# Optimization experiments

Hardware: AMD Instinct MI355X
Metric: run time of the kernel (lower is better)

Reference implementation:

```python
import jax, jax.numpy as jnp
import numpy as np

H = 16  # headNum
D = 1024  # d_model
DK = D // H


def setup_inputs() -> dict:
    key = jax.random.key(0)
    ks = jax.random.split(key, 11)
    B, S = 2, 2048
    scale = 1.0 / np.sqrt(D)
    inp = {
        'query': jax.random.normal(ks[0], (B, S, D), jnp.float32),
        'key':   jax.random.normal(ks[1], (B, S, D), jnp.float32),
        'value': jax.random.normal(ks[2], (B, S, D), jnp.float32),
        # nn.Linear params: W is [out, in], y = x @ W.T + b
        'Wq': jax.random.normal(ks[3], (D, D), jnp.float32) * scale,
        'bq': jnp.zeros((D,), jnp.float32),
        'Wk': jax.random.normal(ks[4], (D, D), jnp.float32) * scale,
        'bk': jnp.zeros((D,), jnp.float32),
        'Wv': jax.random.normal(ks[5], (D, D), jnp.float32) * scale,
        'bv': jnp.zeros((D,), jnp.float32),
        'Wo': jax.random.normal(ks[6], (D, D), jnp.float32) * scale,
        'bo': jnp.zeros((D,), jnp.float32),
    }
    return inp


def reference(query, key, value, Wq, bq, Wk, bk, Wv, bv, Wo, bo):
    B, S, _ = query.shape
    # projections (torch Linear: x @ W.T + b), split heads -> [B, H, S, DK]
    q = (query @ Wq.T + bq).reshape(B, S, H, DK).transpose(0, 2, 1, 3)
    k = (key   @ Wk.T + bk).reshape(B, S, H, DK).transpose(0, 2, 1, 3)
    v = (value @ Wv.T + bv).reshape(B, S, H, DK).transpose(0, 2, 1, 3)
    # scores [B, H, S, S] = Q K^T / sqrt(d_k)  (fully materialized, as in source)
    scores = jnp.einsum('bhqd,bhkd->bhqk', q, k) * (DK ** -0.5)
    p_attn = jax.nn.softmax(scores, axis=-1)  # dropout = identity (eval)
    x = jnp.einsum('bhqk,bhkd->bhqd', p_attn, v)
    x = x.transpose(0, 2, 1, 3).reshape(B, S, H * DK)
    return x @ Wo.T + bo
```

## Files before the change

kernel.cpp:

```cpp
#include <hip/hip_runtime.h>

#define BATCH 2
#define SEQ   2048
#define NH    16
#define DK    64
#define DM    1024
#define MROWS 4096
#define NX    4194304
#define NW    1048576

typedef __attribute__((ext_vector_type(8))) short bf16x8;
typedef __attribute__((ext_vector_type(4))) short bf16x4;
typedef __attribute__((ext_vector_type(4))) float f32x4;
typedef __attribute__((ext_vector_type(4))) unsigned short us16x4;
typedef __attribute__((ext_vector_type(2))) unsigned int u32x2;

#if __has_builtin(__builtin_amdgcn_mfma_f32_16x16x16bf16_1k)
#define MFMA16(a, b, c) __builtin_amdgcn_mfma_f32_16x16x16bf16_1k(a, b, c, 0, 0, 0)
#else
#define MFMA16(a, b, c) (c)
#endif

__device__ __forceinline__ unsigned short f2bf(float f) {
  unsigned int u = __builtin_bit_cast(unsigned int, f);
  u += 0x7FFFu + ((u >> 16) & 1u);
  return (unsigned short)(u >> 16);
}

__device__ __forceinline__ unsigned int pkbf(float hi, float lo) {
#if __has_builtin(__builtin_amdgcn_perm)
  return __builtin_amdgcn_perm(__builtin_bit_cast(unsigned int, hi),
                               __builtin_bit_cast(unsigned int, lo), 0x07060302u);
#else
  return (__builtin_bit_cast(unsigned int, hi) & 0xffff0000u) |
         (__builtin_bit_cast(unsigned int, lo) >> 16);
#endif
}

__device__ __forceinline__ void g2l16(void* lds, const void* g) {
  __builtin_amdgcn_global_load_lds(
      (const __attribute__((address_space(1))) void*)g,
      (__attribute__((address_space(3))) void*)lds, 16, 0, 0);
}

__global__ __launch_bounds__(256) void cast_all(
    const float* __restrict__ q, const float* __restrict__ k, const float* __restrict__ v,
    const float* __restrict__ wq, const float* __restrict__ wk,
    const float* __restrict__ wv, const float* __restrict__ wo,
    unsigned short* __restrict__ dst) {
  size_t e = ((size_t)blockIdx.x * 256 + threadIdx.x) * 4;
  const float* src;
  if      (e < (size_t)NX)        src = q  + e;
  else if (e < (size_t)2*NX)      src = k  + (e - (size_t)NX);
  else if (e < (size_t)3*NX)      src = v  + (e - (size_t)2*NX);
  else if (e < (size_t)3*NX+NW)   src = wq + (e - (size_t)3*NX);
  else if (e < (size_t)3*NX+2*NW) src = wk + (e - (size_t)3*NX-NW);
  else if (e < (size_t)3*NX+3*NW) src = wv + (e - (size_t)3*NX-2*NW);
  else                            src = wo + (e - (size_t)3*NX-3*NW);
  float4 f = *(const float4*)src;
  us16x4 o;
  o[0] = f2bf(f.x); o[1] = f2bf(f.y); o[2] = f2bf(f.z); o[3] = f2bf(f.w);
  *(us16x4*)(dst + e) = o;
}

template <int MODE, int BM>
__global__ __launch_bounds__(256) void gemm_bt(
    const unsigned short* __restrict__ Xbase, const unsigned short* __restrict__ Wbase,
    const float* __restrict__ b0, const float* __restrict__ b1, const float* __restrict__ b2,
    unsigned short* __restrict__ qkv_dst, float* __restrict__ fout, float qscale) {
  constexpr int IM = BM / 32;
  constexpr int ASHOTS = (BM * 32) / 2048;
  const int tid  = threadIdx.x;
  const int lane = tid & 63;
  const int w    = tid >> 6;
  const int wm   = w >> 1, wn = w & 1;
  const int x15  = lane & 15, quad = lane >> 4;
  const int row0 = blockIdx.x * BM;
  const int col0 = blockIdx.y * 128;
  const int z    = blockIdx.z;

  const unsigned short* A  = Xbase + (size_t)z * NX;
  const unsigned short* Wp = Wbase + (size_t)z * NW;
  const float* bias = (MODE == 0) ? (z == 0 ? b0 : (z == 1 ? b1 : b2)) : b0;
  const float zs = (MODE == 0 && z == 0) ? qscale : 1.0f;

  __shared__ __align__(16) unsigned short At[2][BM * 32];
  __shared__ __align__(16) unsigned short Bt[2][128 * 32];

  f32x4 acc[IM][4] = {};

  auto stage = [&](int buf, int kt) {
#pragma unroll
    for (int j = 0; j < ASHOTS; ++j) {
      int e = (j * 256 + tid) * 8;
      int r = e >> 5, c = e & 31;
      g2l16(&At[buf][e], A + (size_t)(row0 + r) * DM + kt + c);
    }
#pragma unroll
    for (int j = 0; j < 2; ++j) {
      int e = (j * 256 + tid) * 8;
      int r = e >> 5, c = e & 31;
      g2l16(&Bt[buf][e], Wp + (size_t)(col0 + r) * DM + kt + c);
    }
  };

  stage(0, 0);
  for (int it = 0; it < DM / 32; ++it) {
    const int cur = it & 1;
    __syncthreads();
    if (it + 1 < DM / 32) stage(cur ^ 1, (it + 1) * 32);
    bf16x8 af[IM], bfv[4];
#pragma unroll
    for (int i = 0; i < IM; ++i)
      af[i] = *(const bf16x8*)&At[cur][(wm * (BM / 2) + i * 16 + x15) * 32 + quad * 8];
#pragma unroll
    for (int jn = 0; jn < 4; ++jn)
      bfv[jn] = *(const bf16x8*)&Bt[cur][(wn * 64 + jn * 16 + x15) * 32 + quad * 8];
#pragma unroll
    for (int i = 0; i < IM; ++i)
#pragma unroll
      for (int jn = 0; jn < 4; ++jn)
        acc[i][jn] = __builtin_amdgcn_mfma_f32_16x16x32_bf16(af[i], bfv[jn], acc[i][jn], 0, 0, 0);
  }

#pragma unroll
  for (int jn = 0; jn < 4; ++jn) {
    const int n = col0 + wn * 64 + jn * 16 + x15;
    const float bv = bias[n];
#pragma unroll
    for (int i = 0; i < IM; ++i) {
      const int m0 = row0 + wm * (BM / 2) + i * 16 + quad * 4;
      if (MODE == 0 && z == 2) {
        us16x4 pk;
#pragma unroll
        for (int r = 0; r < 4; ++r) pk[r] = f2bf(acc[i][jn][r] + bv);
        const int b = m0 >> 11, s = m0 & 2047;
        const int h = n >> 6,  dk = n & 63;
        *(us16x4*)&qkv_dst[(size_t)2 * NX + (((size_t)(b * NH + h) * DK + dk) << 11) + s] = pk;
      } else {
#pragma unroll
        for (int r = 0; r < 4; ++r) {
          const int m = m0 + r;
          float val = (acc[i][jn][r] + bv) * zs;
          if (MODE == 0) {
            const int b = m >> 11, s = m & 2047;
            const int h = n >> 6,  dk = n & 63;
            qkv_dst[(size_t)z * NX + (((size_t)(b * NH + h) * SEQ + s) << 6) + dk] = f2bf(val);
          } else {
            fout[(size_t)m * DM + n] = val;
          }
        }
      }
    }
  }
}

__global__ __launch_bounds__(256) void attn(
    const unsigned short* __restrict__ Qb, const unsigned short* __restrict__ Kb,
    const unsigned short* __restrict__ VTb, unsigned short* __restrict__ AO) {
  const int tid  = threadIdx.x;
  const int lane = tid & 63;
  const int w    = tid >> 6;
  const int x15  = lane & 15, quad = lane >> 4;
  const int qt = blockIdx.x;
  const int h  = blockIdx.y;
  const int b  = blockIdx.z;
  const size_t bh = ((size_t)(b * NH + h)) * SEQ * DK;
  const unsigned short* Q  = Qb  + bh;
  const unsigned short* K  = Kb  + bh;
  const unsigned short* VT = VTb + bh;
  const int q0 = qt * 64 + w * 16;

  __shared__ __align__(16) unsigned short Kl[2][64 * 64];
  __shared__ __align__(16) unsigned short Vl[2][64 * 64];

  bf16x8 qf[2];
#pragma unroll
  for (int ks = 0; ks < 2; ++ks)
    qf[ks] = *(const bf16x8*)&Q[(size_t)(q0 + x15) * DK + ks * 32 + quad * 8];

  f32x4 po[4] = {};
  f32x4 pol = {};
  const bf16x4 vone = {(short)0x3F80, (short)0x3F80, (short)0x3F80, (short)0x3F80};

  const int sK0 = tid >> 3,          sK1 = (tid + 256) >> 3;
  const int dgK0 = (tid & 7) ^ (sK0 & 7), dgK1 = (tid & 7) ^ (sK1 & 7);

  auto stageKV = [&](int buf, int s0) {
    g2l16(&Kl[buf][(size_t)tid * 8],         K + (size_t)(s0 + sK0) * DK + dgK0 * 8);
    g2l16(&Kl[buf][(size_t)(tid + 256) * 8], K + (size_t)(s0 + sK1) * DK + dgK1 * 8);
    g2l16(&Vl[buf][(size_t)tid * 8],         VT + (size_t)sK0 * SEQ + s0 + dgK0 * 8);
    g2l16(&Vl[buf][(size_t)(tid + 256) * 8], VT + (size_t)sK1 * SEQ + s0 + dgK1 * 8);
  };

  stageKV(0, 0);
  for (int s0 = 0; s0 < SEQ; s0 += 64) {
    const int cur = (s0 >> 6) & 1;
    __syncthreads();
    if (s0 + 64 < SEQ) stageKV(cur ^ 1, s0 + 64);

    bf16x8 kf[4][2];
#pragma unroll
    for (int sh = 0; sh < 4; ++sh) {
      const int kbase = (sh * 16 + x15) * 8;
      kf[sh][0] = *(const bf16x8*)&Kl[cur][(kbase + ((0 + quad) ^ (x15 & 7))) * 8];
      kf[sh][1] = *(const bf16x8*)&Kl[cur][(kbase + ((4 + quad) ^ (x15 & 7))) * 8];
    }

#pragma unroll
    for (int sh = 0; sh < 4; ++sh) {
      f32x4 sacc = {};
      sacc = __builtin_amdgcn_mfma_f32_16x16x32_bf16(kf[sh][0], qf[0], sacc, 0, 0, 0);
      sacc = __builtin_amdgcn_mfma_f32_16x16x32_bf16(kf[sh][1], qf[1], sacc, 0, 0, 0);
      float p0 = __builtin_amdgcn_exp2f(sacc[0]);
      float p1 = __builtin_amdgcn_exp2f(sacc[1]);
      float p2 = __builtin_amdgcn_exp2f(sacc[2]);
      float p3 = __builtin_amdgcn_exp2f(sacc[3]);
      u32x2 uu;
      uu[0] = pkbf(p1, p0);
      uu[1] = pkbf(p3, p2);
      bf16x4 pf = __builtin_bit_cast(bf16x4, uu);
      pol = MFMA16(vone, pf, pol);

#pragma unroll
      for (int nt = 0; nt < 4; ++nt) {
        const int d = nt * 16 + x15;
        const int sg = (sh * 2 + (quad >> 1)) ^ (d & 7);
        bf16x4 vf = *(const bf16x4*)&Vl[cur][(d * 8 + sg) * 8 + (quad & 1) * 4];
        po[nt] = MFMA16(vf, pf, po[nt]);
      }
    }
  }

  const float inv = 1.0f / pol[0];
  const int s = q0 + x15;
#pragma unroll
  for (int nt = 0; nt < 4; ++nt) {
    us16x4 pk;
#pragma unroll
    for (int r = 0; r < 4; ++r) pk[r] = f2bf(po[nt][r] * inv);
    const int d = nt * 16 + quad * 4;
    *(us16x4*)&AO[((size_t)(b * SEQ + s)) * DM + h * DK + d] = pk;
  }
}

extern "C" void kernel_launch(void* const* d_in, const int* in_sizes, int n_in,
                              void* d_out, int out_size, void* d_ws, size_t ws_size,
                              hipStream_t stream) {
  const float* q  = (const float*)d_in[0];
  const float* k  = (const float*)d_in[1];
  const float* v  = (const float*)d_in[2];
  const float* wq = (const float*)d_in[3];
  const float* bq = (const float*)d_in[4];
  const float* wk = (const float*)d_in[5];
  const float* bk = (const float*)d_in[6];
  const float* wv = (const float*)d_in[7];
  const float* bv = (const float*)d_in[8];
  const float* wo = (const float*)d_in[9];
  const float* bo = (const float*)d_in[10];
  float* out = (float*)d_out;

  unsigned short* ws = (unsigned short*)d_ws;
  unsigned short* Xq = ws;
  unsigned short* Wb = ws + (size_t)3 * NX;
  unsigned short* Qb = ws + (size_t)3 * NX + 4 * NW;
  unsigned short* AO = Qb + (size_t)3 * NX;

  const float qscale = 0.125f * 1.4426950408889634f;

  cast_all<<<16384, 256, 0, stream>>>(q, k, v, wq, wk, wv, wo, ws);
  gemm_bt<0, 128><<<dim3(32, 8, 3), 256, 0, stream>>>(Xq, Wb, bq, bk, bv, Qb, nullptr, qscale);
  attn<<<dim3(32, 16, 2), 256, 0, stream>>>(Qb, Qb + (size_t)NX, Qb + (size_t)2 * NX, AO);
  gemm_bt<1, 64><<<dim3(64, 8, 1), 256, 0, stream>>>(AO, Wb + (size_t)3 * NW, bo, bo, bo,
                                                     nullptr, out, 1.0f);
}
```

Measured before the change: 234.0 us.

## Fuse fp32-to-bf16 activation cast into QKV GEMM A-tile staging

The separate cast of query/key/value to bf16 is removed. The QKV projection GEMM now reads fp32 activations into registers, converts them with a packed bf16 convert, and writes them into LDS after the MFMA block, so the next tile's load overlaps compute. This avoids writing and re-reading about 24MB of bf16 activations in an extra pass, at the cost of register-staged loads in place of direct global-to-LDS loads, and double the global A traffic per tile. The attention kernel also precomputes its swizzled LDS offsets to cut per-iteration index arithmetic.

```diff
diff --git a/kernel.cpp b/kernel.cpp
--- a/kernel.cpp
+++ b/kernel.cpp
@@ -27,6 +27,16 @@
   return (unsigned short)(u >> 16);
 }
 
+__device__ __forceinline__ unsigned int cvt2bf(float a, float b) {
+#if __has_builtin(__builtin_amdgcn_cvt_pk_bf16_f32)
+  typedef __attribute__((ext_vector_type(2))) __bf16 bf16v2;
+  bf16v2 v = __builtin_amdgcn_cvt_pk_bf16_f32(a, b);
+  return __builtin_bit_cast(unsigned int, v);
+#else
+  return (unsigned int)f2bf(a) | ((unsigned int)f2bf(b) << 16);
+#endif
+}
+
 __device__ __forceinline__ unsigned int pkbf(float hi, float lo) {
 #if __has_builtin(__builtin_amdgcn_perm)
   return __builtin_amdgcn_perm(__builtin_bit_cast(unsigned int, hi),
@@ -43,56 +53,143 @@
       (__attribute__((address_space(3))) void*)lds, 16, 0, 0);
 }
 
-__global__ __launch_bounds__(256) void cast_all(
-    const float* __restrict__ q, const float* __restrict__ k, const float* __restrict__ v,
+__global__ __launch_bounds__(256) void cast_w(
     const float* __restrict__ wq, const float* __restrict__ wk,
     const float* __restrict__ wv, const float* __restrict__ wo,
     unsigned short* __restrict__ dst) {
   size_t e = ((size_t)blockIdx.x * 256 + threadIdx.x) * 4;
   const float* src;
-  if      (e < (size_t)NX)        src = q  + e;
-  else if (e < (size_t)2*NX)      src = k  + (e - (size_t)NX);
-  else if (e < (size_t)3*NX)      src = v  + (e - (size_t)2*NX);
-  else if (e < (size_t)3*NX+NW)   src = wq + (e - (size_t)3*NX);
-  else if (e < (size_t)3*NX+2*NW) src = wk + (e - (size_t)3*NX-NW);
-  else if (e < (size_t)3*NX+3*NW) src = wv + (e - (size_t)3*NX-2*NW);
-  else                            src = wo + (e - (size_t)3*NX-3*NW);
+  if      (e < (size_t)NW)     src = wq + e;
+  else if (e < (size_t)2*NW)   src = wk + (e - (size_t)NW);
+  else if (e < (size_t)3*NW)   src = wv + (e - (size_t)2*NW);
+  else                         src = wo + (e - (size_t)3*NW);
   float4 f = *(const float4*)src;
   us16x4 o;
   o[0] = f2bf(f.x); o[1] = f2bf(f.y); o[2] = f2bf(f.z); o[3] = f2bf(f.w);
   *(us16x4*)(dst + e) = o;
 }
 
-template <int MODE, int BM>
-__global__ __launch_bounds__(256) void gemm_bt(
-    const unsigned short* __restrict__ Xbase, const unsigned short* __restrict__ Wbase,
-    const float* __restrict__ b0, const float* __restrict__ b1, const float* __restrict__ b2,
-    unsigned short* __restrict__ qkv_dst, float* __restrict__ fout, float qscale) {
-  constexpr int IM = BM / 32;
-  constexpr int ASHOTS = (BM * 32) / 2048;
+__global__ __launch_bounds__(256) void gemm_qkv(
+    const float* __restrict__ Xq, const float* __restrict__ Xk, const float* __restrict__ Xv,
+    const unsigned short* __restrict__ Wb,
+    const float* __restrict__ bq, const float* __restrict__ bk, const float* __restrict__ bv,
+    unsigned short* __restrict__ dst, float qscale) {
   const int tid  = threadIdx.x;
   const int lane = tid & 63;
   const int w    = tid >> 6;
   const int wm   = w >> 1, wn = w & 1;
   const int x15  = lane & 15, quad = lane >> 4;
-  const int row0 = blockIdx.x * BM;
+  const int row0 = blockIdx.x * 128;
   const int col0 = blockIdx.y * 128;
   const int z    = blockIdx.z;
 
-  const unsigned short* A  = Xbase + (size_t)z * NX;
-  const unsigned short* Wp = Wbase + (size_t)z * NW;
-  const float* bias = (MODE == 0) ? (z == 0 ? b0 : (z == 1 ? b1 : b2)) : b0;
-  const float zs = (MODE == 0 && z == 0) ? qscale : 1.0f;
-
-  __shared__ __align__(16) unsigned short At[2][BM * 32];
+  const float* X = (z == 0) ? Xq : (z == 1 ? Xk : Xv);
+  const unsigned short* Wp = Wb + (size_t)z * NW;
+  const float* bias = (z == 0) ? bq : (z == 1 ? bk : bv);
+  const float zs = (z == 0) ? qscale : 1.0f;
+
+  __shared__ __align__(16) unsigned short At[2][128 * 32];
   __shared__ __align__(16) unsigned short Bt[2][128 * 32];
 
-  f32x4 acc[IM][4] = {};
+  f32x4 acc[4][4] = {};
+  float4 xa[4];
+
+  auto loadA = [&](int kt) {
+#pragma unroll
+    for (int j = 0; j < 4; ++j) {
+      int e = (j * 256 + tid) * 4;
+      int r = e >> 5, c = e & 31;
+      xa[j] = *(const float4*)&X[(size_t)(row0 + r) * DM + kt + c];
+    }
+  };
+  auto writeA = [&](int buf) {
+#pragma unroll
+    for (int j = 0; j < 4; ++j) {
+      int e = (j * 256 + tid) * 4;
+      u32x2 p;
+      p[0] = cvt2bf(xa[j].x, xa[j].y);
+      p[1] = cvt2bf(xa[j].z, xa[j].w);
+      *(u32x2*)&At[buf][e] = p;
+    }
+  };
+  auto stageB = [&](int buf, int kt) {
+#pragma unroll
+    for (int j = 0; j < 2; ++j) {
+      int e = (j * 256 + tid) * 8;
+      int r = e >> 5, c = e & 31;
+      g2l16(&Bt[buf][e], Wp + (size_t)(col0 + r) * DM + kt + c);
+    }
+  };
+
+  loadA(0);
+  stageB(0, 0);
+  writeA(0);
+  for (int it = 0; it < DM / 32; ++it) {
+    const int cur = it & 1;
+    __syncthreads();
+    const bool nxt = (it + 1 < DM / 32);
+    if (nxt) { loadA((it + 1) * 32); stageB(cur ^ 1, (it + 1) * 32); }
+    bf16x8 af[4], bfv[4];
+#pragma unroll
+    for (int i = 0; i < 4; ++i) {
+      af[i]  = *(const bf16x8*)&At[cur][(wm * 64 + i * 16 + x15) * 32 + quad * 8];
+      bfv[i] = *(const bf16x8*)&Bt[cur][(wn * 64 + i * 16 + x15) * 32 + quad * 8];
+    }
+#pragma unroll
+    for (int i = 0; i < 4; ++i)
+#pragma unroll
+      for (int jn = 0; jn < 4; ++jn)
+        acc[i][jn] = __builtin_amdgcn_mfma_f32_16x16x32_bf16(af[i], bfv[jn], acc[i][jn], 0, 0, 0);
+    if (nxt) writeA(cur ^ 1);
+  }
+
+#pragma unroll
+  for (int jn = 0; jn < 4; ++jn) {
+    const int n = col0 + wn * 64 + jn * 16 + x15;
+    const float bv = bias[n];
+#pragma unroll
+    for (int i = 0; i < 4; ++i) {
+      const int m0 = row0 + wm * 64 + i * 16 + quad * 4;
+      if (z == 2) {
+        us16x4 pk;
+#pragma unroll
+        for (int r = 0; r < 4; ++r) pk[r] = f2bf(acc[i][jn][r] + bv);
+        const int b = m0 >> 11, s = m0 & 2047;
+        const int h = n >> 6,  dk = n & 63;
+        *(us16x4*)&dst[(size_t)2 * NX + (((size_t)(b * NH + h) * DK + dk) << 11) + s] = pk;
+      } else {
+#pragma unroll
+        for (int r = 0; r < 4; ++r) {
+          const int m = m0 + r;
+          float val = (acc[i][jn][r] + bv) * zs;
+          const int b = m >> 11, s = m & 2047;
+          const int h = n >> 6,  dk = n & 63;
+          dst[(size_t)z * NX + (((size_t)(b * NH + h) * SEQ + s) << 6) + dk] = f2bf(val);
+        }
+      }
+    }
+  }
+}
+
+__global__ __launch_bounds__(256) void gemm_out(
+    const unsigned short* __restrict__ A, const unsigned short* __restrict__ Wp,
+    const float* __restrict__ bias, float* __restrict__ fout) {
+  const int tid  = threadIdx.x;
+  const int lane = tid & 63;
+  const int w    = tid >> 6;
+  const int wm   = w >> 1, wn = w & 1;
+  const int x15  = lane & 15, quad = lane >> 4;
+  const int row0 = blockIdx.x * 64;
+  const int col0 = blockIdx.y * 128;
+
+  __shared__ __align__(16) unsigned short At[2][64 * 32];
+  __shared__ __align__(16) unsigned short Bt[2][128 * 32];
+
+  f32x4 acc[2][4] = {};
 
   auto stage = [&](int buf, int kt) {
-#pragma unroll
-    for (int j = 0; j < ASHOTS; ++j) {
-      int e = (j * 256 + tid) * 8;
+    {
+      int e = tid * 8;
       int r = e >> 5, c = e & 31;
       g2l16(&At[buf][e], A + (size_t)(row0 + r) * DM + kt + c);
     }
@@ -109,15 +206,15 @@
     const int cur = it & 1;
     __syncthreads();
     if (it + 1 < DM / 32) stage(cur ^ 1, (it + 1) * 32);
-    bf16x8 af[IM], bfv[4];
-#pragma unroll
-    for (int i = 0; i < IM; ++i)
-      af[i] = *(const bf16x8*)&At[cur][(wm * (BM / 2) + i * 16 + x15) * 32 + quad * 8];
+    bf16x8 af[2], bfv[4];
+#pragma unroll
+    for (int i = 0; i < 2; ++i)
+      af[i] = *(const bf16x8*)&At[cur][(wm * 32 + i * 16 + x15) * 32 + quad * 8];
 #pragma unroll
     for (int jn = 0; jn < 4; ++jn)
       bfv[jn] = *(const bf16x8*)&Bt[cur][(wn * 64 + jn * 16 + x15) * 32 + quad * 8];
 #pragma unroll
-    for (int i = 0; i < IM; ++i)
+    for (int i = 0; i < 2; ++i)
 #pragma unroll
       for (int jn = 0; jn < 4; ++jn)
         acc[i][jn] = __builtin_amdgcn_mfma_f32_16x16x32_bf16(af[i], bfv[jn], acc[i][jn], 0, 0, 0);
@@ -128,29 +225,11 @@
     const int n = col0 + wn * 64 + jn * 16 + x15;
     const float bv = bias[n];
 #pragma unroll
-    for (int i = 0; i < IM; ++i) {
-      const int m0 = row0 + wm * (BM / 2) + i * 16 + quad * 4;
-      if (MODE == 0 && z == 2) {
-        us16x4 pk;
-#pragma unroll
-        for (int r = 0; r < 4; ++r) pk[r] = f2bf(acc[i][jn][r] + bv);
-        const int b = m0 >> 11, s = m0 & 2047;
-        const int h = n >> 6,  dk = n & 63;
-        *(us16x4*)&qkv_dst[(size_t)2 * NX + (((size_t)(b * NH + h) * DK + dk) << 11) + s] = pk;
-      } else {
-#pragma unroll
-        for (int r = 0; r < 4; ++r) {
-          const int m = m0 + r;
-          float val = (acc[i][jn][r] + bv) * zs;
-          if (MODE == 0) {
-            const int b = m >> 11, s = m & 2047;
-            const int h = n >> 6,  dk = n & 63;
-            qkv_dst[(size_t)z * NX + (((size_t)(b * NH + h) * SEQ + s) << 6) + dk] = f2bf(val);
-          } else {
-            fout[(size_t)m * DM + n] = val;
-          }
-        }
-      }
+    for (int i = 0; i < 2; ++i) {
+      const int m0 = row0 + wm * 32 + i * 16 + quad * 4;
+#pragma unroll
+      for (int r = 0; r < 4; ++r)
+        fout[(size_t)(m0 + r) * DM + n] = acc[i][jn][r] + bv;
     }
   }
 }
@@ -183,6 +262,15 @@
   f32x4 pol = {};
   const bf16x4 vone = {(short)0x3F80, (short)0x3F80, (short)0x3F80, (short)0x3F80};
 
+  const int kb0 = x15 * 64 + (quad ^ (x15 & 7)) * 8;
+  const int kb1 = kb0 ^ 32;
+  int vb[4];
+#pragma unroll
+  for (int nt = 0; nt < 4; ++nt) {
+    const int d = nt * 16 + x15;
+    vb[nt] = d * 64 + (((quad >> 1) ^ (d & 7)) * 8) + (quad & 1) * 4;
+  }
+
   const int sK0 = tid >> 3,          sK1 = (tid + 256) >> 3;
   const int dgK0 = (tid & 7) ^ (sK0 & 7), dgK1 = (tid & 7) ^ (sK1 & 7);
 
@@ -199,12 +287,14 @@
     __syncthreads();
     if (s0 + 64 < SEQ) stageKV(cur ^ 1, s0 + 64);
 
+    const unsigned short* Klc = &Kl[cur][0];
+    const unsigned short* Vlc = &Vl[cur][0];
+
     bf16x8 kf[4][2];
 #pragma unroll
     for (int sh = 0; sh < 4; ++sh) {
-      const int kbase = (sh * 16 + x15) * 8;
-      kf[sh][0] = *(const bf16x8*)&Kl[cur][(kbase + ((0 + quad) ^ (x15 & 7))) * 8];
-      kf[sh][1] = *(const bf16x8*)&Kl[cur][(kbase + ((4 + quad) ^ (x15 & 7))) * 8];
+      kf[sh][0] = *(const bf16x8*)&Klc[kb0 + sh * 1024];
+      kf[sh][1] = *(const bf16x8*)&Klc[kb1 + sh * 1024];
     }
 
 #pragma unroll
@@ -224,9 +314,7 @@
 
 #pragma unroll
       for (int nt = 0; nt < 4; ++nt) {
-        const int d = nt * 16 + x15;
-        const int sg = (sh * 2 + (quad >> 1)) ^ (d & 7);
-        bf16x4 vf = *(const bf16x4*)&Vl[cur][(d * 8 + sg) * 8 + (quad & 1) * 4];
+        bf16x4 vf = *(const bf16x4*)&Vlc[vb[nt] ^ (sh * 16)];
         po[nt] = MFMA16(vf, pf, po[nt]);
       }
     }
@@ -261,16 +349,14 @@
   float* out = (float*)d_out;
 
   unsigned short* ws = (unsigned short*)d_ws;
-  unsigned short* Xq = ws;
-  unsigned short* Wb = ws + (size_t)3 * NX;
-  unsigned short* Qb = ws + (size_t)3 * NX + 4 * NW;
+  unsigned short* Wb = ws;
+  unsigned short* Qb = ws + (size_t)4 * NW;
   unsigned short* AO = Qb + (size_t)3 * NX;
 
   const float qscale = 0.125f * 1.4426950408889634f;
 
-  cast_all<<<16384, 256, 0, stream>>>(q, k, v, wq, wk, wv, wo, ws);
-  gemm_bt<0, 128><<<dim3(32, 8, 3), 256, 0, stream>>>(Xq, Wb, bq, bk, bv, Qb, nullptr, qscale);
+  cast_w<<<4096, 256, 0, stream>>>(wq, wk, wv, wo, Wb);
+  gemm_qkv<<<dim3(32, 8, 3), 256, 0, stream>>>(q, k, v, Wb, bq, bk, bv, Qb, qscale);
   attn<<<dim3(32, 16, 2), 256, 0, stream>>>(Qb, Qb + (size_t)NX, Qb + (size_t)2 * NX, AO);
-  gemm_bt<1, 64><<<dim3(64, 8, 1), 256, 0, stream>>>(AO, Wb + (size_t)3 * NW, bo, bo, bo,
-                                                     nullptr, out, 1.0f);
-}
+  gemm_out<<<dim3(64, 8, 1), 256, 0, stream>>>(AO, Wb + (size_t)3 * NW, bo, out);
+}
```

New measurement: 234.3 us. Within noise of the previous version (+0.1%).
